# Kernel tuning notes

Hardware: AMD Instinct MI355X
Metric: run time of the kernel (lower is better)

## Reference

```python
import jax, jax.numpy as jnp
import numpy as np

D_MODEL = 1024
BATCH = 8
SEQ = 2048
LN_EPS = 1e-5


def setup_inputs() -> dict:
    key = jax.random.key(0)
    ks = jax.random.split(key, 8)
    scale = 0.1 / np.sqrt(D_MODEL)
    x = jax.random.normal(ks[0], (BATCH, SEQ, D_MODEL), dtype=jnp.float32)
    return {
        "x": x,
        "ln_w": jnp.ones((D_MODEL,), jnp.float32),
        "ln_b": jnp.zeros((D_MODEL,), jnp.float32),
        # layer_idx=0, n_layers=4 -> ratio_1 = 1.0 (init), perturb slightly for a non-trivial mix
        "tmk": jnp.ones((D_MODEL,), jnp.float32) * 0.9,
        "tmv": jnp.ones((D_MODEL,), jnp.float32) * 0.9,
        "tmr": jnp.ones((D_MODEL,), jnp.float32) * 0.9,
        "decay_w": jnp.full((D_MODEL,), -0.5, jnp.float32)
        + 0.1 * jax.random.normal(ks[1], (D_MODEL,), jnp.float32),
        "Wk": scale * jax.random.normal(ks[2], (D_MODEL, D_MODEL), jnp.float32),
        "Wv": scale * jax.random.normal(ks[3], (D_MODEL, D_MODEL), jnp.float32),
        "Wr": scale * jax.random.normal(ks[4], (D_MODEL, D_MODEL), jnp.float32),
        "Wo": scale * jax.random.normal(ks[5], (D_MODEL, D_MODEL), jnp.float32),
    }


def _layernorm(z, w, b):
    m = jnp.mean(z, axis=-1, keepdims=True)
    v = jnp.mean(jnp.square(z - m), axis=-1, keepdims=True)
    return (z - m) * jax.lax.rsqrt(v + LN_EPS) * w + b


def reference(x, ln_w, ln_b, tmk, tmv, tmr, decay_w, Wk, Wv, Wr, Wo):
    # x: (B, T, D)
    xn = _layernorm(x, ln_w, ln_b)
    # prev_x at t=0 is zeros (not LN of zeros), afterwards LN(x_{t-1})
    prev = jnp.pad(xn[:, :-1, :], ((0, 0), (1, 0), (0, 0)))
    xk = xn * tmk + prev * (1.0 - tmk)
    xv = xn * tmv + prev * (1.0 - tmv)
    xr = xn * tmr + prev * (1.0 - tmr)
    k = jnp.einsum("btd,ed->bte", xk, Wk)
    v = jnp.einsum("btd,ed->bte", xv, Wv)
    r = jax.nn.sigmoid(jnp.einsum("btd,ed->bte", xr, Wr))
    decay = jax.nn.sigmoid(decay_w)  # (D,)

    kv = (k * v).swapaxes(0, 1)  # (T, B, D) time-major for scan

    def step(S, kv_t):
        S_new = decay * S + kv_t
        return S_new, S_new

    S0 = jnp.zeros((x.shape[0], x.shape[2]), x.dtype)
    final_S, S_seq = jax.lax.scan(step, S0, kv)
    S_seq = S_seq.swapaxes(0, 1)  # (B, T, D)

    out = x + r * jnp.einsum("btd,ed->bte", S_seq, Wo)
    return out, final_S, S_seq
```

## Files before the change

### kernel.cpp

```cpp
#include <hip/hip_runtime.h>
#include <cstdint>

#define D_MODEL 1024
#define SEQ 2048
#define BATCH 8
#define M_TOTAL (BATCH*SEQ)
#define NC 64
#define CL (SEQ/NC)

typedef float f32x4 __attribute__((ext_vector_type(4)));
typedef short bf16x8 __attribute__((ext_vector_type(8)));
typedef unsigned short u16x4 __attribute__((ext_vector_type(4)));

__device__ __forceinline__ float b2f(unsigned short s){
  union { float f; unsigned u; } z; z.u = ((unsigned)s) << 16; return z.f;
}
__device__ __forceinline__ unsigned short f2b(float f){
  union { float f; unsigned u; } z; z.f = f;
  unsigned u = z.u;
  u += 0x7fffu + ((u >> 16) & 1u);
  return (unsigned short)(u >> 16);
}
__device__ __forceinline__ float sigmoidf_(float v){
  return 1.0f / (1.0f + __expf(-v));
}
__device__ __forceinline__ void gld_lds16(const void* g, void* l){
  __builtin_amdgcn_global_load_lds((const __attribute__((address_space(1))) unsigned int*)g,
                                   (__attribute__((address_space(3))) unsigned int*)l,
                                   16, 0, 0);
}

__device__ __forceinline__ void swz256(int bid, int& m0, int& n0){
  int xcd = bid & 7;
  int loc = bid >> 3;
  int wg  = xcd*32 + loc;
  m0 = (wg >> 2) * 256;
  n0 = (wg & 3) * 256;
}

__global__ __launch_bounds__(256) void wconv_kernel(const float* __restrict__ W0, const float* __restrict__ W1,
                                                    const float* __restrict__ W2, const float* __restrict__ W3,
                                                    unsigned short* __restrict__ WC){
  int mat = blockIdx.y;
  const float* src = (mat==0) ? W0 : (mat==1) ? W1 : (mat==2) ? W2 : W3;
  size_t i = ((size_t)blockIdx.x*256 + threadIdx.x)*4;
  f32x4 v = *(const f32x4*)(src + i);
  u16x4 o; o[0]=f2b(v[0]); o[1]=f2b(v[1]); o[2]=f2b(v[2]); o[3]=f2b(v[3]);
  *(u16x4*)(WC + (size_t)mat*1048576 + i) = o;
}

__global__ __launch_bounds__(256) void lnmix_kernel(const float* __restrict__ x,
                                                    const float* __restrict__ lnw, const float* __restrict__ lnb,
                                                    const float* __restrict__ tmk, const float* __restrict__ tmv,
                                                    const float* __restrict__ tmr,
                                                    unsigned short* __restrict__ XK, unsigned short* __restrict__ XV,
                                                    unsigned short* __restrict__ XR){
  int r0 = blockIdx.x * 8;
  int tid = threadIdx.x;
  bool seqfirst = (r0 & (SEQ-1)) == 0;
  size_t col = (size_t)tid*4;

  f32x4 xr[9];
  float s1[9], s2[9];
  #pragma unroll
  for (int i=0;i<9;i++){
    if (i==0 && seqfirst){
      xr[0][0]=0.f; xr[0][1]=0.f; xr[0][2]=0.f; xr[0][3]=0.f;
    } else {
      xr[i] = *(const f32x4*)(x + (size_t)(r0-1+i)*D_MODEL + col);
    }
    s1[i] = xr[i][0]+xr[i][1]+xr[i][2]+xr[i][3];
    s2[i] = xr[i][0]*xr[i][0]+xr[i][1]*xr[i][1]+xr[i][2]*xr[i][2]+xr[i][3]*xr[i][3];
  }
  #pragma unroll
  for (int off = 32; off > 0; off >>= 1){
    #pragma unroll
    for (int i=0;i<9;i++){
      s1[i] += __shfl_xor(s1[i], off);
      s2[i] += __shfl_xor(s2[i], off);
    }
  }
  __shared__ float red[4][18];
  int w = tid >> 6, lane = tid & 63;
  if (lane == 0){
    #pragma unroll
    for (int i=0;i<9;i++){ red[w][i]=s1[i]; red[w][9+i]=s2[i]; }
  }
  __syncthreads();
  float mean[9], rstd[9];
  #pragma unroll
  for (int i=0;i<9;i++){
    float a = red[0][i]+red[1][i]+red[2][i]+red[3][i];
    float b = red[0][9+i]+red[1][9+i]+red[2][9+i]+red[3][9+i];
    mean[i] = a*(1.0f/1024.0f);
    float var = b*(1.0f/1024.0f) - mean[i]*mean[i];
    rstd[i] = rsqrtf(var + 1e-5f);
  }

  f32x4 wv = *(const f32x4*)(lnw + col);
  f32x4 bv = *(const f32x4*)(lnb + col);
  f32x4 k4 = *(const f32x4*)(tmk + col);
  f32x4 v4 = *(const f32x4*)(tmv + col);
  f32x4 r4 = *(const f32x4*)(tmr + col);

  f32x4 np;
  if (seqfirst){ np[0]=0.f; np[1]=0.f; np[2]=0.f; np[3]=0.f; }
  else {
    #pragma unroll
    for (int j=0;j<4;j++) np[j] = (xr[0][j]-mean[0])*rstd[0]*wv[j] + bv[j];
  }
  #pragma unroll
  for (int i=0;i<8;i++){
    f32x4 nc;
    #pragma unroll
    for (int j=0;j<4;j++) nc[j] = (xr[i+1][j]-mean[i+1])*rstd[i+1]*wv[j] + bv[j];
    u16x4 ok, ov, orr;
    #pragma unroll
    for (int j=0;j<4;j++){
      ok[j]  = f2b(np[j] + k4[j]*(nc[j]-np[j]));
      ov[j]  = f2b(np[j] + v4[j]*(nc[j]-np[j]));
      orr[j] = f2b(np[j] + r4[j]*(nc[j]-np[j]));
    }
    size_t base = (size_t)(r0+i)*D_MODEL + col;
    *(u16x4*)(XK + base) = ok;
    *(u16x4*)(XV + base) = ov;
    *(u16x4*)(XR + base) = orr;
    np = nc;
  }
}

__device__ __forceinline__ void gemm256_core(const unsigned short* __restrict__ A,
                                             const unsigned short* __restrict__ W,
                                             int m0, int n0, int tid,
                                             unsigned short* As, unsigned short* Bs,
                                             f32x4 (&acc)[8][4]){
  int wid = tid >> 6, lane = tid & 63;
  int wm = wid >> 2, wn = wid & 3;
  int fr = lane & 15, fg = lane >> 4;

  int offAg[4], offBg[4], offL[4];
  #pragma unroll
  for (int it = 0; it < 4; ++it){
    int chunk = it*512 + tid;
    int row = chunk >> 3;
    int cg = (chunk & 7) ^ (row & 7);
    offAg[it] = (m0+row)*D_MODEL + cg*8;
    offBg[it] = (n0+row)*D_MODEL + cg*8;
    offL[it]  = chunk*8;
  }

  #define STAGE(bsel, kt_) { \
    _Pragma("unroll") \
    for (int it = 0; it < 4; ++it){ \
      gld_lds16(A + offAg[it] + (kt_)*64, &As[(bsel)*16384 + offL[it]]); \
      gld_lds16(W + offBg[it] + (kt_)*64, &Bs[(bsel)*16384 + offL[it]]); \
    } }

  STAGE(0, 0);
  STAGE(1, 1);
  asm volatile("s_waitcnt vmcnt(8)" ::: "memory");
  __builtin_amdgcn_s_barrier();

  bf16x8 aL[4][2], aH[4][2], bL[2][2], bH[2][2];

  #pragma unroll 1
  for (int kt = 0; kt < 16; ++kt){
    const unsigned short* Ab = &As[(kt & 1)*16384];
    const unsigned short* Bb = &Bs[(kt & 1)*16384];

    #pragma unroll
    for (int mi=0; mi<4; ++mi)
      #pragma unroll
      for (int ks=0; ks<2; ++ks){
        int r = wm*128 + mi*16 + fr;
        aL[mi][ks] = *(const bf16x8*)(&Ab[r*64 + (((ks*4+fg)^(r&7))<<3)]);
      }
    #pragma unroll
    for (int ni=0; ni<2; ++ni)
      #pragma unroll
      for (int ks=0; ks<2; ++ks){
        int r = wn*64 + ni*16 + fr;
        bL[ni][ks] = *(const bf16x8*)(&Bb[r*64 + (((ks*4+fg)^(r&7))<<3)]);
      }
    __builtin_amdgcn_s_barrier();
    asm volatile("s_waitcnt lgkmcnt(0)" ::: "memory");
    __builtin_amdgcn_s_setprio(1);
    #pragma unroll
    for (int mi=0; mi<4; ++mi)
      #pragma unroll
      for (int ni=0; ni<2; ++ni)
        #pragma unroll
        for (int ks=0; ks<2; ++ks)
          acc[mi][ni] = __builtin_amdgcn_mfma_f32_16x16x32_bf16(aL[mi][ks], bL[ni][ks], acc[mi][ni], 0, 0, 0);
    __builtin_amdgcn_s_setprio(0);
    __builtin_amdgcn_s_barrier();

    #pragma unroll
    for (int ni=0; ni<2; ++ni)
      #pragma unroll
      for (int ks=0; ks<2; ++ks){
        int r = wn*64 + (ni+2)*16 + fr;
        bH[ni][ks] = *(const bf16x8*)(&Bb[r*64 + (((ks*4+fg)^(r&7))<<3)]);
      }
    __builtin_amdgcn_s_barrier();
    asm volatile("s_waitcnt lgkmcnt(0)" ::: "memory");
    __builtin_amdgcn_s_setprio(1);
    #pragma unroll
    for (int mi=0; mi<4; ++mi)
      #pragma unroll
      for (int ni=0; ni<2; ++ni)
        #pragma unroll
        for (int ks=0; ks<2; ++ks)
          acc[mi][ni+2] = __builtin_amdgcn_mfma_f32_16x16x32_bf16(aL[mi][ks], bH[ni][ks], acc[mi][ni+2], 0, 0, 0);
    __builtin_amdgcn_s_setprio(0);
    __builtin_amdgcn_s_barrier();

    #pragma unroll
    for (int mi=0; mi<4; ++mi)
      #pragma unroll
      for (int ks=0; ks<2; ++ks){
        int r = wm*128 + (mi+4)*16 + fr;
        aH[mi][ks] = *(const bf16x8*)(&Ab[r*64 + (((ks*4+fg)^(r&7))<<3)]);
      }
    asm volatile("s_waitcnt lgkmcnt(0)" ::: "memory");
    __builtin_amdgcn_s_barrier();
    asm volatile("" ::: "memory");
    __builtin_amdgcn_s_setprio(1);
    #pragma unroll
    for (int mi=0; mi<4; ++mi)
      #pragma unroll
      for (int ni=0; ni<2; ++ni)
        #pragma unroll
        for (int ks=0; ks<2; ++ks)
          acc[mi+4][ni+2] = __builtin_amdgcn_mfma_f32_16x16x32_bf16(aH[mi][ks], bH[ni][ks], acc[mi+4][ni+2], 0, 0, 0);
    __builtin_amdgcn_s_setprio(0);

    if (kt < 14) STAGE((kt & 1), kt+2);
    __builtin_amdgcn_s_setprio(1);
    #pragma unroll
    for (int mi=0; mi<4; ++mi)
      #pragma unroll
      for (int ni=0; ni<2; ++ni)
        #pragma unroll
        for (int ks=0; ks<2; ++ks)
          acc[mi+4][ni] = __builtin_amdgcn_mfma_f32_16x16x32_bf16(aH[mi][ks], bL[ni][ks], acc[mi+4][ni], 0, 0, 0);
    __builtin_amdgcn_s_setprio(0);
    if (kt < 14)       asm volatile("s_waitcnt vmcnt(8)" ::: "memory");
    else if (kt == 14) asm volatile("s_waitcnt vmcnt(0)" ::: "memory");
    if (kt < 15){
      __builtin_amdgcn_s_barrier();
      asm volatile("" ::: "memory");
    }
  }
  #undef STAGE
}

__global__ __launch_bounds__(512) void gemm_kr_kernel(const unsigned short* __restrict__ XK,
                                                      const unsigned short* __restrict__ XR,
                                                      const unsigned short* __restrict__ Wk,
                                                      const unsigned short* __restrict__ Wr,
                                                      unsigned short* __restrict__ KB,
                                                      unsigned short* __restrict__ RB){
  __shared__ alignas(16) unsigned short As[2*16384];
  __shared__ alignas(16) unsigned short Bs[2*16384];
  int m0, n0; swz256(blockIdx.x, m0, n0);
  int z = blockIdx.z;
  int tid = threadIdx.x;
  const unsigned short* A = z ? XR : XK;
  const unsigned short* W = z ? Wr : Wk;
  unsigned short* O       = z ? RB : KB;

  f32x4 acc[8][4];
  #pragma unroll
  for (int i=0;i<8;i++)
    #pragma unroll
    for (int j=0;j<4;j++){ acc[i][j][0]=0.f; acc[i][j][1]=0.f; acc[i][j][2]=0.f; acc[i][j][3]=0.f; }

  gemm256_core(A, W, m0, n0, tid, As, Bs, acc);

  int wid = tid >> 6, lane = tid & 63;
  int wm = wid >> 2, wn = wid & 3;
  int fr = lane & 15, fg = lane >> 4;
  #pragma unroll
  for (int mi=0; mi<8; ++mi){
    #pragma unroll
    for (int ni=0; ni<4; ++ni){
      int c = n0 + wn*64 + ni*16 + fr;
      #pragma unroll
      for (int j=0; j<4; ++j){
        int r = m0 + wm*128 + mi*16 + fg*4 + j;
        size_t idx = (size_t)r*D_MODEL + c;
        float val = acc[mi][ni][j];
        if (z) val = sigmoidf_(val);
        O[idx] = f2b(val);
      }
    }
  }
}

__global__ __launch_bounds__(512) void gemm_v_kernel(const unsigned short* __restrict__ XV,
                                                     const unsigned short* __restrict__ Wv,
                                                     unsigned short* __restrict__ KB){
  __shared__ alignas(16) unsigned short As[2*16384];
  __shared__ alignas(16) unsigned short Bs[2*16384];
  int m0, n0; swz256(blockIdx.x, m0, n0);
  int tid = threadIdx.x;

  f32x4 acc[8][4];
  #pragma unroll
  for (int i=0;i<8;i++)
    #pragma unroll
    for (int j=0;j<4;j++){ acc[i][j][0]=0.f; acc[i][j][1]=0.f; acc[i][j][2]=0.f; acc[i][j][3]=0.f; }

  gemm256_core(XV, Wv, m0, n0, tid, As, Bs, acc);

  int wid = tid >> 6, lane = tid & 63;
  int wm = wid >> 2, wn = wid & 3;
  int fr = lane & 15, fg = lane >> 4;
  #pragma unroll
  for (int mi=0; mi<8; ++mi){
    #pragma unroll
    for (int ni=0; ni<4; ++ni){
      int c = n0 + wn*64 + ni*16 + fr;
      #pragma unroll
      for (int j=0; j<4; ++j){
        int r = m0 + wm*128 + mi*16 + fg*4 + j;
        size_t idx = (size_t)r*D_MODEL + c;
        KB[idx] = f2b(acc[mi][ni][j] * b2f(KB[idx]));
      }
    }
  }
}

__global__ __launch_bounds__(512) void gemm_out_kernel(const unsigned short* __restrict__ Sb,
                                                       const unsigned short* __restrict__ Wo,
                                                       const float* __restrict__ x,
                                                       const unsigned short* __restrict__ RB,
                                                       float* __restrict__ out){
  __shared__ alignas(16) unsigned short As[2*16384];
  __shared__ alignas(16) unsigned short Bs[2*16384];
  int m0, n0; swz256(blockIdx.x, m0, n0);
  int tid = threadIdx.x;

  f32x4 acc[8][4];
  #pragma unroll
  for (int i=0;i<8;i++)
    #pragma unroll
    for (int j=0;j<4;j++){ acc[i][j][0]=0.f; acc[i][j][1]=0.f; acc[i][j][2]=0.f; acc[i][j][3]=0.f; }

  gemm256_core(Sb, Wo, m0, n0, tid, As, Bs, acc);

  int wid = tid >> 6, lane = tid & 63;
  int wm = wid >> 2, wn = wid & 3;
  int fr = lane & 15, fg = lane >> 4;
  #pragma unroll
  for (int mi=0; mi<8; ++mi){
    #pragma unroll
    for (int ni=0; ni<4; ++ni){
      int c = n0 + wn*64 + ni*16 + fr;
      #pragma unroll
      for (int j=0; j<4; ++j){
        int r = m0 + wm*128 + mi*16 + fg*4 + j;
        size_t idx = (size_t)r*D_MODEL + c;
        float rr = b2f(RB[idx]);
        out[idx] = x[idx] + rr * acc[mi][ni][j];
      }
    }
  }
}

__global__ __launch_bounds__(256) void scan_p1_kernel(const unsigned short* __restrict__ kv,
                                                      const float* __restrict__ dw,
                                                      float* __restrict__ carr){
  int bc = blockIdx.x;
  int b = bc >> 6, c = bc & (NC-1);
  int d0 = threadIdx.x * 4;
  float dx = sigmoidf_(dw[d0+0]);
  float dy = sigmoidf_(dw[d0+1]);
  float dz = sigmoidf_(dw[d0+2]);
  float dwv = sigmoidf_(dw[d0+3]);
  float Sx=0.f, Sy=0.f, Sz=0.f, Sw=0.f;
  size_t base = ((size_t)(b*SEQ + c*CL))*D_MODEL + d0;
  for (int i=0;i<CL;i++){
    u16x4 k4 = *(const u16x4*)(kv + base);
    Sx = dx*Sx + b2f(k4[0]);
    Sy = dy*Sy + b2f(k4[1]);
    Sz = dz*Sz + b2f(k4[2]);
    Sw = dwv*Sw + b2f(k4[3]);
    base += D_MODEL;
  }
  f32x4 o; o[0]=Sx; o[1]=Sy; o[2]=Sz; o[3]=Sw;
  *(f32x4*)(carr + (size_t)bc*D_MODEL + d0) = o;
}

__global__ __launch_bounds__(256) void scan_p2_kernel(const float* __restrict__ dw, float* __restrict__ carr){
  int gid = blockIdx.x*256 + threadIdx.x;
  int b = gid >> 10, d = gid & (D_MODEL-1);
  float dec = sigmoidf_(dw[d]);
  float dL = dec;
  #pragma unroll
  for (int i=0;i<5;i++) dL *= dL;
  float S = 0.f;
  for (int c=0;c<NC;c++){
    size_t idx = ((size_t)(b*NC + c))*D_MODEL + d;
    float cr = carr[idx];
    carr[idx] = S;
    S = dL*S + cr;
  }
}

__global__ __launch_bounds__(256) void scan_p3_kernel(const unsigned short* __restrict__ kv,
                                                      const float* __restrict__ dw,
                                                      const float* __restrict__ cin,
                                                      float* __restrict__ sseq,
                                                      float* __restrict__ finalS,
                                                      unsigned short* __restrict__ sb16){
  int bc = blockIdx.x;
  int b = bc >> 6, c = bc & (NC-1);
  int d0 = threadIdx.x * 4;
  float dx = sigmoidf_(dw[d0+0]);
  float dy = sigmoidf_(dw[d0+1]);
  float dz = sigmoidf_(dw[d0+2]);
  float dwv = sigmoidf_(dw[d0+3]);
  f32x4 S = *(const f32x4*)(cin + (size_t)bc*D_MODEL + d0);
  size_t base = ((size_t)(b*SEQ + c*CL))*D_MODEL + d0;
  for (int i=0;i<CL;i++){
    u16x4 k4 = *(const u16x4*)(kv + base);
    S[0] = dx*S[0] + b2f(k4[0]);
    S[1] = dy*S[1] + b2f(k4[1]);
    S[2] = dz*S[2] + b2f(k4[2]);
    S[3] = dwv*S[3] + b2f(k4[3]);
    *(f32x4*)(sseq + base) = S;
    u16x4 s4; s4[0]=f2b(S[0]); s4[1]=f2b(S[1]); s4[2]=f2b(S[2]); s4[3]=f2b(S[3]);
    *(u16x4*)(sb16 + base) = s4;
    base += D_MODEL;
  }
  if (c == NC-1)
    *(f32x4*)(finalS + (size_t)b*D_MODEL + d0) = S;
}

extern "C" void kernel_launch(void* const* d_in, const int* in_sizes, int n_in,
                              void* d_out, int out_size, void* d_ws, size_t ws_size,
                              hipStream_t stream){
  const float* x   = (const float*)d_in[0];
  const float* lnw = (const float*)d_in[1];
  const float* lnb = (const float*)d_in[2];
  const float* tmk = (const float*)d_in[3];
  const float* tmv = (const float*)d_in[4];
  const float* tmr = (const float*)d_in[5];
  const float* dw  = (const float*)d_in[6];
  const float* Wk  = (const float*)d_in[7];
  const float* Wv  = (const float*)d_in[8];
  const float* Wr  = (const float*)d_in[9];
  const float* Wo  = (const float*)d_in[10];

  float* out    = (float*)d_out;
  float* finalS = out + (size_t)M_TOTAL*D_MODEL;
  float* sseq   = finalS + (size_t)BATCH*D_MODEL;

  unsigned short* XK = (unsigned short*)d_out;
  unsigned short* XV = (unsigned short*)((char*)d_out + 33554432);
  unsigned short* XR = (unsigned short*)sseq;

  char* w = (char*)d_ws;
  unsigned short* WC   = (unsigned short*)(w + 0);
  unsigned short* SB16 = (unsigned short*)(w + 8388608);
  unsigned short* KB   = (unsigned short*)(w + 41943040);
  unsigned short* RB   = (unsigned short*)(w + 75497472);
  float*          CARR = (float*)(w + 109051904);

  wconv_kernel<<<dim3(1024,4), 256, 0, stream>>>(Wk, Wv, Wr, Wo, WC);
  lnmix_kernel<<<M_TOTAL/8, 256, 0, stream>>>(x, lnw, lnb, tmk, tmv, tmr, XK, XV, XR);

  gemm_kr_kernel<<<dim3(256,1,2), 512, 0, stream>>>(XK, XR, WC, WC + (size_t)2*1048576, KB, RB);
  gemm_v_kernel<<<256, 512, 0, stream>>>(XV, WC + (size_t)1048576, KB);

  scan_p1_kernel<<<BATCH*NC, 256, 0, stream>>>(KB, dw, CARR);
  scan_p2_kernel<<<32, 256, 0, stream>>>(dw, CARR);
  scan_p3_kernel<<<BATCH*NC, 256, 0, stream>>>(KB, dw, CARR, sseq, finalS, SB16);

  gemm_out_kernel<<<256, 512, 0, stream>>>(SB16, WC + (size_t)3*1048576, x, RB, out);
}
```

Measured before the change: 266.1 us.

## Shrink GEMM tiles to 256x128 single-buffered with two blocks per CU

The three GEMM kernels move from 512-thread blocks on 256x256 tiles with double-buffered LDS to 256-thread blocks on 256x128 tiles with a single LDS buffer. Launch bounds ask for two blocks per CU, and the grid doubles to match, with an updated XCD swizzle. The aim is to overlap one block's global-load latency with the other block's MFMA work instead of relying on in-block double buffering. The cost is a full vmcnt(0) wait plus a barrier every k-step, and more reloading of A because the N tiles are narrower.

```diff
diff --git a/kernel.cpp b/kernel.cpp
--- a/kernel.cpp
+++ b/kernel.cpp
@@ -30,12 +30,12 @@
                                    16, 0, 0);
 }
 
-__device__ __forceinline__ void swz256(int bid, int& m0, int& n0){
+__device__ __forceinline__ void swz_mn(int bid, int& m0, int& n0){
   int xcd = bid & 7;
   int loc = bid >> 3;
-  int wg  = xcd*32 + loc;
-  m0 = (wg >> 2) * 256;
-  n0 = (wg & 3) * 256;
+  int wg  = xcd*64 + loc;
+  m0 = (wg >> 3) * 256;
+  n0 = (wg & 7) * 128;
 }
 
 __global__ __launch_bounds__(256) void wconv_kernel(const float* __restrict__ W0, const float* __restrict__ W1,
@@ -135,52 +135,57 @@
                                              unsigned short* As, unsigned short* Bs,
                                              f32x4 (&acc)[8][4]){
   int wid = tid >> 6, lane = tid & 63;
-  int wm = wid >> 2, wn = wid & 3;
+  int wm = wid >> 1, wn = wid & 1;
   int fr = lane & 15, fg = lane >> 4;
 
-  int offAg[4], offBg[4], offL[4];
-  #pragma unroll
-  for (int it = 0; it < 4; ++it){
-    int chunk = it*512 + tid;
+  int offAg[8], offBg[4];
+  #pragma unroll
+  for (int it = 0; it < 8; ++it){
+    int chunk = it*256 + tid;
     int row = chunk >> 3;
     int cg = (chunk & 7) ^ (row & 7);
     offAg[it] = (m0+row)*D_MODEL + cg*8;
+  }
+  #pragma unroll
+  for (int it = 0; it < 4; ++it){
+    int chunk = it*256 + tid;
+    int row = chunk >> 3;
+    int cg = (chunk & 7) ^ (row & 7);
     offBg[it] = (n0+row)*D_MODEL + cg*8;
-    offL[it]  = chunk*8;
-  }
-
-  #define STAGE(bsel, kt_) { \
+  }
+
+  #define STAGE(kt_) { \
     _Pragma("unroll") \
-    for (int it = 0; it < 4; ++it){ \
-      gld_lds16(A + offAg[it] + (kt_)*64, &As[(bsel)*16384 + offL[it]]); \
-      gld_lds16(W + offBg[it] + (kt_)*64, &Bs[(bsel)*16384 + offL[it]]); \
-    } }
-
-  STAGE(0, 0);
-  STAGE(1, 1);
-  asm volatile("s_waitcnt vmcnt(8)" ::: "memory");
-  __builtin_amdgcn_s_barrier();
+    for (int it = 0; it < 8; ++it) \
+      gld_lds16(A + offAg[it] + (kt_)*64, &As[(it*256+tid)*8]); \
+    _Pragma("unroll") \
+    for (int it = 0; it < 4; ++it) \
+      gld_lds16(W + offBg[it] + (kt_)*64, &Bs[(it*256+tid)*8]); \
+  }
+
+  STAGE(0);
 
   bf16x8 aL[4][2], aH[4][2], bL[2][2], bH[2][2];
 
   #pragma unroll 1
   for (int kt = 0; kt < 16; ++kt){
-    const unsigned short* Ab = &As[(kt & 1)*16384];
-    const unsigned short* Bb = &Bs[(kt & 1)*16384];
+    asm volatile("s_waitcnt vmcnt(0)" ::: "memory");
+    __builtin_amdgcn_s_barrier();
+    asm volatile("" ::: "memory");
 
     #pragma unroll
     for (int mi=0; mi<4; ++mi)
       #pragma unroll
       for (int ks=0; ks<2; ++ks){
         int r = wm*128 + mi*16 + fr;
-        aL[mi][ks] = *(const bf16x8*)(&Ab[r*64 + (((ks*4+fg)^(r&7))<<3)]);
+        aL[mi][ks] = *(const bf16x8*)(&As[r*64 + (((ks*4+fg)^(r&7))<<3)]);
       }
     #pragma unroll
     for (int ni=0; ni<2; ++ni)
       #pragma unroll
       for (int ks=0; ks<2; ++ks){
         int r = wn*64 + ni*16 + fr;
-        bL[ni][ks] = *(const bf16x8*)(&Bb[r*64 + (((ks*4+fg)^(r&7))<<3)]);
+        bL[ni][ks] = *(const bf16x8*)(&Bs[r*64 + (((ks*4+fg)^(r&7))<<3)]);
       }
     __builtin_amdgcn_s_barrier();
     asm volatile("s_waitcnt lgkmcnt(0)" ::: "memory");
@@ -200,7 +205,7 @@
       #pragma unroll
       for (int ks=0; ks<2; ++ks){
         int r = wn*64 + (ni+2)*16 + fr;
-        bH[ni][ks] = *(const bf16x8*)(&Bb[r*64 + (((ks*4+fg)^(r&7))<<3)]);
+        bH[ni][ks] = *(const bf16x8*)(&Bs[r*64 + (((ks*4+fg)^(r&7))<<3)]);
       }
     __builtin_amdgcn_s_barrier();
     asm volatile("s_waitcnt lgkmcnt(0)" ::: "memory");
@@ -220,11 +225,14 @@
       #pragma unroll
       for (int ks=0; ks<2; ++ks){
         int r = wm*128 + (mi+4)*16 + fr;
-        aH[mi][ks] = *(const bf16x8*)(&Ab[r*64 + (((ks*4+fg)^(r&7))<<3)]);
+        aH[mi][ks] = *(const bf16x8*)(&As[r*64 + (((ks*4+fg)^(r&7))<<3)]);
       }
     asm volatile("s_waitcnt lgkmcnt(0)" ::: "memory");
     __builtin_amdgcn_s_barrier();
     asm volatile("" ::: "memory");
+
+    if (kt < 15) STAGE(kt+1);
+
     __builtin_amdgcn_s_setprio(1);
     #pragma unroll
     for (int mi=0; mi<4; ++mi)
@@ -233,10 +241,6 @@
         #pragma unroll
         for (int ks=0; ks<2; ++ks)
           acc[mi+4][ni+2] = __builtin_amdgcn_mfma_f32_16x16x32_bf16(aH[mi][ks], bH[ni][ks], acc[mi+4][ni+2], 0, 0, 0);
-    __builtin_amdgcn_s_setprio(0);
-
-    if (kt < 14) STAGE((kt & 1), kt+2);
-    __builtin_amdgcn_s_setprio(1);
     #pragma unroll
     for (int mi=0; mi<4; ++mi)
       #pragma unroll
@@ -245,25 +249,19 @@
         for (int ks=0; ks<2; ++ks)
           acc[mi+4][ni] = __builtin_amdgcn_mfma_f32_16x16x32_bf16(aH[mi][ks], bL[ni][ks], acc[mi+4][ni], 0, 0, 0);
     __builtin_amdgcn_s_setprio(0);
-    if (kt < 14)       asm volatile("s_waitcnt vmcnt(8)" ::: "memory");
-    else if (kt == 14) asm volatile("s_waitcnt vmcnt(0)" ::: "memory");
-    if (kt < 15){
-      __builtin_amdgcn_s_barrier();
-      asm volatile("" ::: "memory");
-    }
   }
   #undef STAGE
 }
 
-__global__ __launch_bounds__(512) void gemm_kr_kernel(const unsigned short* __restrict__ XK,
-                                                      const unsigned short* __restrict__ XR,
-                                                      const unsigned short* __restrict__ Wk,
-                                                      const unsigned short* __restrict__ Wr,
-                                                      unsigned short* __restrict__ KB,
-                                                      unsigned short* __restrict__ RB){
-  __shared__ alignas(16) unsigned short As[2*16384];
-  __shared__ alignas(16) unsigned short Bs[2*16384];
-  int m0, n0; swz256(blockIdx.x, m0, n0);
+__global__ __launch_bounds__(256, 2) void gemm_kr_kernel(const unsigned short* __restrict__ XK,
+                                                         const unsigned short* __restrict__ XR,
+                                                         const unsigned short* __restrict__ Wk,
+                                                         const unsigned short* __restrict__ Wr,
+                                                         unsigned short* __restrict__ KB,
+                                                         unsigned short* __restrict__ RB){
+  __shared__ alignas(16) unsigned short As[16384];
+  __shared__ alignas(16) unsigned short Bs[8192];
+  int m0, n0; swz_mn(blockIdx.x, m0, n0);
   int z = blockIdx.z;
   int tid = threadIdx.x;
   const unsigned short* A = z ? XR : XK;
@@ -279,7 +277,7 @@
   gemm256_core(A, W, m0, n0, tid, As, Bs, acc);
 
   int wid = tid >> 6, lane = tid & 63;
-  int wm = wid >> 2, wn = wid & 3;
+  int wm = wid >> 1, wn = wid & 1;
   int fr = lane & 15, fg = lane >> 4;
   #pragma unroll
   for (int mi=0; mi<8; ++mi){
@@ -298,12 +296,12 @@
   }
 }
 
-__global__ __launch_bounds__(512) void gemm_v_kernel(const unsigned short* __restrict__ XV,
-                                                     const unsigned short* __restrict__ Wv,
-                                                     unsigned short* __restrict__ KB){
-  __shared__ alignas(16) unsigned short As[2*16384];
-  __shared__ alignas(16) unsigned short Bs[2*16384];
-  int m0, n0; swz256(blockIdx.x, m0, n0);
+__global__ __launch_bounds__(256, 2) void gemm_v_kernel(const unsigned short* __restrict__ XV,
+                                                        const unsigned short* __restrict__ Wv,
+                                                        unsigned short* __restrict__ KB){
+  __shared__ alignas(16) unsigned short As[16384];
+  __shared__ alignas(16) unsigned short Bs[8192];
+  int m0, n0; swz_mn(blockIdx.x, m0, n0);
   int tid = threadIdx.x;
 
   f32x4 acc[8][4];
@@ -315,7 +313,7 @@
   gemm256_core(XV, Wv, m0, n0, tid, As, Bs, acc);
 
   int wid = tid >> 6, lane = tid & 63;
-  int wm = wid >> 2, wn = wid & 3;
+  int wm = wid >> 1, wn = wid & 1;
   int fr = lane & 15, fg = lane >> 4;
   #pragma unroll
   for (int mi=0; mi<8; ++mi){
@@ -332,14 +330,14 @@
   }
 }
 
-__global__ __launch_bounds__(512) void gemm_out_kernel(const unsigned short* __restrict__ Sb,
-                                                       const unsigned short* __restrict__ Wo,
-                                                       const float* __restrict__ x,
-                                                       const unsigned short* __restrict__ RB,
-                                                       float* __restrict__ out){
-  __shared__ alignas(16) unsigned short As[2*16384];
-  __shared__ alignas(16) unsigned short Bs[2*16384];
-  int m0, n0; swz256(blockIdx.x, m0, n0);
+__global__ __launch_bounds__(256, 2) void gemm_out_kernel(const unsigned short* __restrict__ Sb,
+                                                          const unsigned short* __restrict__ Wo,
+                                                          const float* __restrict__ x,
+                                                          const unsigned short* __restrict__ RB,
+                                                          float* __restrict__ out){
+  __shared__ alignas(16) unsigned short As[16384];
+  __shared__ alignas(16) unsigned short Bs[8192];
+  int m0, n0; swz_mn(blockIdx.x, m0, n0);
   int tid = threadIdx.x;
 
   f32x4 acc[8][4];
@@ -351,7 +349,7 @@
   gemm256_core(Sb, Wo, m0, n0, tid, As, Bs, acc);
 
   int wid = tid >> 6, lane = tid & 63;
-  int wm = wid >> 2, wn = wid & 3;
+  int wm = wid >> 1, wn = wid & 1;
   int fr = lane & 15, fg = lane >> 4;
   #pragma unroll
   for (int mi=0; mi<8; ++mi){
@@ -472,12 +470,12 @@
   wconv_kernel<<<dim3(1024,4), 256, 0, stream>>>(Wk, Wv, Wr, Wo, WC);
   lnmix_kernel<<<M_TOTAL/8, 256, 0, stream>>>(x, lnw, lnb, tmk, tmv, tmr, XK, XV, XR);
 
-  gemm_kr_kernel<<<dim3(256,1,2), 512, 0, stream>>>(XK, XR, WC, WC + (size_t)2*1048576, KB, RB);
-  gemm_v_kernel<<<256, 512, 0, stream>>>(XV, WC + (size_t)1048576, KB);
+  gemm_kr_kernel<<<dim3(512,1,2), 256, 0, stream>>>(XK, XR, WC, WC + (size_t)2*1048576, KB, RB);
+  gemm_v_kernel<<<512, 256, 0, stream>>>(XV, WC + (size_t)1048576, KB);
 
   scan_p1_kernel<<<BATCH*NC, 256, 0, stream>>>(KB, dw, CARR);
   scan_p2_kernel<<<32, 256, 0, stream>>>(dw, CARR);
   scan_p3_kernel<<<BATCH*NC, 256, 0, stream>>>(KB, dw, CARR, sseq, finalS, SB16);
 
-  gemm_out_kernel<<<256, 512, 0, stream>>>(SB16, WC + (size_t)3*1048576, x, RB, out);
-}
+  gemm_out_kernel<<<512, 256, 0, stream>>>(SB16, WC + (size_t)3*1048576, x, RB, out);
+}
```

After: 248.9 us. -6.5%, faster.
